# Optimization experiments

Hardware: AMD Instinct MI355X
Metric: run time of the kernel (lower is better)

## Reference

```python
import jax, jax.numpy as jnp
import numpy as np

B, S, H = 64, 2048, 512


def setup_inputs() -> dict:
    key = jax.random.key(0)
    ks = jax.random.split(key, 11)
    sc = 1.0 / np.sqrt(H)
    return {
        "encoder_output": jax.random.normal(ks[0], (B, S, H), jnp.float32),
        "decoder_hidden": jax.random.normal(ks[1], (B, H), jnp.float32),
        "coverage": jax.random.uniform(ks[2], (B, S), jnp.float32),
        # params (torch Linear: y = x @ W.T + b); we store W already transposed as [in, out]
        "Wh": jax.random.normal(ks[3], (H, H), jnp.float32) * sc,
        "bh": jax.random.normal(ks[4], (H,), jnp.float32) * sc,
        "Ws": jax.random.normal(ks[5], (H, H), jnp.float32) * sc,
        "bs": jax.random.normal(ks[6], (H,), jnp.float32) * sc,
        "Wc": jax.random.normal(ks[7], (1, H), jnp.float32) * sc,  # Linear(1, H)
        "bc": jax.random.normal(ks[8], (H,), jnp.float32) * sc,
        "v_w": jax.random.normal(ks[9], (H,), jnp.float32) * sc,   # Linear(H, 1) weight
        "v_b": jax.random.normal(ks[10], (1,), jnp.float32) * sc,
    }


def reference(encoder_output, decoder_hidden, coverage, Wh, bh, Ws, bs, Wc, bc, v_w, v_b):
    # encoder_feature: [B,S,H]
    enc_f = jnp.einsum('bsh,hk->bsk', encoder_output, Wh) + bh
    # decoder_feature: [B,1,H]
    dec_f = (decoder_hidden @ Ws + bs)[:, None, :]
    # coverage_feature: [B,S,H] = cov[...,None] @ Wc(1,H) + bc
    cov_f = coverage[:, :, None] * Wc[0] + bc
    feat = jnp.tanh(enc_f + dec_f + cov_f)          # [B,S,H]
    e_t = jnp.einsum('bsh,h->bs', feat, v_w) + v_b[0]  # [B,S]
    a_t = jax.nn.softmax(e_t, axis=-1)
    sum_coverage = coverage + a_t
    return a_t, sum_coverage
```

## Files before the change

kernel.cpp:

```cpp
#include <hip/hip_runtime.h>
#include <math.h>


#define B_ 64
#define S_ 2048
#define H_ 512
#define M_ (B_ * S_)

#define RPB 128
#define BN 64
#define NPH 8

typedef __attribute__((ext_vector_type(4))) float f32x4;
typedef __attribute__((ext_vector_type(8))) short s16x8;

__device__ __forceinline__ short f2bf(float f) {
    unsigned u = __float_as_uint(f);
    u += 0x7fffu + ((u >> 16) & 1u);
    return (short)(u >> 16);
}

__device__ __forceinline__ s16x8 cvt8(float4 a, float4 b) {
    s16x8 r;
    r[0] = f2bf(a.x); r[1] = f2bf(a.y); r[2] = f2bf(a.z); r[3] = f2bf(a.w);
    r[4] = f2bf(b.x); r[5] = f2bf(b.y); r[6] = f2bf(b.z); r[7] = f2bf(b.w);
    return r;
}

__device__ __forceinline__ float fast_tanh(float x) {
    return 1.0f - 2.0f / (__expf(2.0f * x) + 1.0f);
}

__global__ __launch_bounds__(256) void transpose_cast(
    const float* __restrict__ Wh, short* __restrict__ Bt) {
    __shared__ float tile[32][33];
    const int n0 = blockIdx.x * 32, k0 = blockIdx.y * 32;
    const int tx = threadIdx.x & 31, ty = threadIdx.x >> 5;
#pragma unroll
    for (int r = 0; r < 32; r += 8)
        tile[ty + r][tx] = Wh[(size_t)(k0 + ty + r) * H_ + n0 + tx];
    __syncthreads();
#pragma unroll
    for (int r = 0; r < 32; r += 8)
        Bt[(size_t)(n0 + ty + r) * H_ + k0 + tx] = f2bf(tile[tx][ty + r]);
}

__global__ __launch_bounds__(512) void dec_kernel(
    const float* __restrict__ dh, const float* __restrict__ Ws,
    const float* __restrict__ bs, const float* __restrict__ bh,
    const float* __restrict__ bc, float* __restrict__ D) {
    const int b = blockIdx.x;
    const int h = threadIdx.x;
    __shared__ float sdh[H_];
    sdh[h] = dh[b * H_ + h];
    __syncthreads();
    float acc = bs[h] + bh[h] + bc[h];
#pragma unroll 8
    for (int k = 0; k < H_; ++k)
        acc = fmaf(sdh[k], Ws[k * H_ + h], acc);
    D[b * H_ + h] = acc;
}

__global__ __launch_bounds__(256, 2) void gemm_fused(
    const float* __restrict__ A,
    const short* __restrict__ Bt,
    const float* __restrict__ cover,
    const float* __restrict__ Wc,
    const float* __restrict__ vw,
    const float* __restrict__ D,
    float* __restrict__ e_t) {
    __shared__ __align__(16) short Bs[BN * H_];

    const int tid = threadIdx.x;
    const int w = tid >> 6;
    const int l = tid & 63;
    const int q = l >> 4;
    const int ml = l & 15;

    const int row_blk = blockIdx.x * RPB;
    const int b = row_blk >> 11;
    const int r0 = row_blk + w * 32;

    s16x8 a[2][16];
    {
        const float* ap = A + (size_t)(r0 + ml) * H_ + q * 8;
#pragma unroll
        for (int kw = 0; kw < 16; ++kw) {
#pragma unroll
            for (int t = 0; t < 2; ++t) {
                const float* p = ap + (size_t)t * 16 * H_ + kw * 32;
                float4 x = *(const float4*)p;
                float4 y = *(const float4*)(p + 4);
                a[t][kw] = cvt8(x, y);
            }
        }
    }

    float cv[2][4];
#pragma unroll
    for (int t = 0; t < 2; ++t)
#pragma unroll
        for (int r = 0; r < 4; ++r)
            cv[t][r] = cover[r0 + t * 16 + q * 4 + r];

    const int sn = tid >> 2;
    const int sq = tid & 3;
    const int sv = sn >> 4;
    const int sml = sn & 15;
    short* sdst0 = Bs + sv * 512 + (sq * 16 + (sml ^ (sq << 1))) * 8;
    const int fb = (q * 16 + (ml ^ (q << 1))) * 8;

    float ecur[2][4] = {};

    for (int ph = 0; ph < NPH; ++ph) {
        const short* sg = Bt + ((size_t)ph * BN + sn) * H_ + sq * 8;
        if (ph) __syncthreads();
#pragma unroll
        for (int hv = 0; hv < 2; ++hv) {
            s16x8 tmp[8];
#pragma unroll
            for (int j = 0; j < 8; ++j)
                tmp[j] = *(const s16x8*)(sg + (hv * 8 + j) * 32);
#pragma unroll
            for (int j = 0; j < 8; ++j)
                *(s16x8*)(sdst0 + (size_t)(hv * 8 + j) * 2048) = tmp[j];
        }
        __syncthreads();

        float wc[4], vv[4], dd[4];
#pragma unroll
        for (int v = 0; v < 4; ++v) {
            const int n = ph * BN + v * 16 + ml;
            wc[v] = Wc[n];
            vv[v] = vw[n];
            dd[v] = D[b * H_ + n];
        }

        f32x4 acc[2][4];
#pragma unroll
        for (int t = 0; t < 2; ++t)
#pragma unroll
            for (int v = 0; v < 4; ++v) acc[t][v] = (f32x4)0.0f;

#pragma unroll
        for (int kw = 0; kw < 16; ++kw) {
            s16x8 bfr[4];
#pragma unroll
            for (int v = 0; v < 4; ++v)
                bfr[v] = *(const s16x8*)&Bs[kw * 2048 + v * 512 + fb];
#pragma unroll
            for (int v = 0; v < 4; ++v) {
                acc[0][v] = __builtin_amdgcn_mfma_f32_16x16x32_bf16(
                    a[0][kw], bfr[v], acc[0][v], 0, 0, 0);
                acc[1][v] = __builtin_amdgcn_mfma_f32_16x16x32_bf16(
                    a[1][kw], bfr[v], acc[1][v], 0, 0, 0);
            }
        }

#pragma unroll
        for (int t = 0; t < 2; ++t) {
#pragma unroll
            for (int v = 0; v < 4; ++v) {
                ecur[t][0] += vv[v] * fast_tanh(acc[t][v].x + fmaf(cv[t][0], wc[v], dd[v]));
                ecur[t][1] += vv[v] * fast_tanh(acc[t][v].y + fmaf(cv[t][1], wc[v], dd[v]));
                ecur[t][2] += vv[v] * fast_tanh(acc[t][v].z + fmaf(cv[t][2], wc[v], dd[v]));
                ecur[t][3] += vv[v] * fast_tanh(acc[t][v].w + fmaf(cv[t][3], wc[v], dd[v]));
            }
        }
    }

#pragma unroll
    for (int t = 0; t < 2; ++t) {
        float p0 = ecur[t][0], p1 = ecur[t][1], p2 = ecur[t][2], p3 = ecur[t][3];
#pragma unroll
        for (int s = 1; s < 16; s <<= 1) {
            p0 += __shfl_xor(p0, s, 64);
            p1 += __shfl_xor(p1, s, 64);
            p2 += __shfl_xor(p2, s, 64);
            p3 += __shfl_xor(p3, s, 64);
        }
        if (ml == 0) {
            float4 st = {p0, p1, p2, p3};
            *(float4*)&e_t[r0 + t * 16 + q * 4] = st;
        }
    }
}

__global__ __launch_bounds__(256) void softmax_kernel(
    const float* __restrict__ e_t, const float* __restrict__ cover,
    const float* __restrict__ vb, float* __restrict__ out) {
    const int b = blockIdx.x;
    const int tid = threadIdx.x;
    const float vbv = vb[0];

    float e[8];
    float mx = -1e30f;
#pragma unroll
    for (int r = 0; r < 8; ++r) {
        e[r] = e_t[b * S_ + r * 256 + tid] + vbv;
        mx = fmaxf(mx, e[r]);
    }
#pragma unroll
    for (int off = 32; off >= 1; off >>= 1) mx = fmaxf(mx, __shfl_xor(mx, off, 64));

    __shared__ float sm[4], ss[4], sbc[2];
    const int wid = tid >> 6, lane = tid & 63;
    if (lane == 0) sm[wid] = mx;
    __syncthreads();
    if (tid == 0) sbc[0] = fmaxf(fmaxf(sm[0], sm[1]), fmaxf(sm[2], sm[3]));
    __syncthreads();
    mx = sbc[0];

    float ex[8];
    float sum = 0.0f;
#pragma unroll
    for (int r = 0; r < 8; ++r) {
        ex[r] = __expf(e[r] - mx);
        sum += ex[r];
    }
#pragma unroll
    for (int off = 32; off >= 1; off >>= 1) sum += __shfl_xor(sum, off, 64);
    if (lane == 0) ss[wid] = sum;
    __syncthreads();
    if (tid == 0) sbc[1] = ss[0] + ss[1] + ss[2] + ss[3];
    __syncthreads();
    const float inv = 1.0f / sbc[1];

#pragma unroll
    for (int r = 0; r < 8; ++r) {
        const int s = r * 256 + tid;
        const float a = ex[r] * inv;
        out[b * S_ + s] = a;
        out[M_ + b * S_ + s] = cover[b * S_ + s] + a;
    }
}

extern "C" void kernel_launch(void* const* d_in, const int* in_sizes, int n_in,
                              void* d_out, int out_size, void* d_ws, size_t ws_size,
                              hipStream_t stream) {
    const float* enc = (const float*)d_in[0];
    const float* dh  = (const float*)d_in[1];
    const float* cov = (const float*)d_in[2];
    const float* Wh  = (const float*)d_in[3];
    const float* bh  = (const float*)d_in[4];
    const float* Ws  = (const float*)d_in[5];
    const float* bs  = (const float*)d_in[6];
    const float* Wc  = (const float*)d_in[7];
    const float* bc  = (const float*)d_in[8];
    const float* vw  = (const float*)d_in[9];
    const float* vb  = (const float*)d_in[10];
    float* out = (float*)d_out;

    float* e_t  = (float*)d_ws;
    float* Dws  = e_t + M_;
    short* Whbt = (short*)(Dws + B_ * H_);

    transpose_cast<<<dim3(H_ / 32, H_ / 32), 256, 0, stream>>>(Wh, Whbt);
    dec_kernel<<<B_, 512, 0, stream>>>(dh, Ws, bs, bh, bc, Dws);
    gemm_fused<<<M_ / RPB, 256, 0, stream>>>(enc, Whbt, cov, Wc, vw, Dws, e_t);
    softmax_kernel<<<B_, 256, 0, stream>>>(e_t, cov, vb, out);
}
```

Baseline: 492.4 us.

## Double-buffer weight tiles via direct global-to-LDS DMA with prearranged layout

The transpose kernel now writes the bf16 weights in the exact per-phase fragment order the MFMA loop reads. The GEMM then streams each 32-column phase straight into LDS with global_load_lds, double-buffered so the next phase loads while the current one computes. Blocks become 8 waves of 16 rows each, with launch bounds of 4 blocks per CU, which cuts A-fragment registers and raises occupancy. The decoder matvec is split across two blocks per batch. In exchange there are twice as many phases, each ending in a barrier, and each B fragment is reused by fewer rows.

```diff
diff --git a/kernel.cpp b/kernel.cpp
--- a/kernel.cpp
+++ b/kernel.cpp
@@ -8,11 +8,13 @@
 #define M_ (B_ * S_)
 
 #define RPB 128
-#define BN 64
-#define NPH 8
+#define BN 32
+#define NPH 16
+#define PHB 32768
 
 typedef __attribute__((ext_vector_type(4))) float f32x4;
 typedef __attribute__((ext_vector_type(8))) short s16x8;
+typedef unsigned int u32;
 
 __device__ __forceinline__ short f2bf(float f) {
     unsigned u = __float_as_uint(f);
@@ -31,8 +33,14 @@
     return 1.0f - 2.0f / (__expf(2.0f * x) + 1.0f);
 }
 
+__device__ __forceinline__ void dma16(const void* g, void* s) {
+    __builtin_amdgcn_global_load_lds(
+        (const __attribute__((address_space(1))) u32*)g,
+        (__attribute__((address_space(3))) u32*)s, 16, 0, 0);
+}
+
 __global__ __launch_bounds__(256) void transpose_cast(
-    const float* __restrict__ Wh, short* __restrict__ Bt) {
+    const float* __restrict__ Wh, short* __restrict__ Bimg) {
     __shared__ float tile[32][33];
     const int n0 = blockIdx.x * 32, k0 = blockIdx.y * 32;
     const int tx = threadIdx.x & 31, ty = threadIdx.x >> 5;
@@ -40,19 +48,27 @@
     for (int r = 0; r < 32; r += 8)
         tile[ty + r][tx] = Wh[(size_t)(k0 + ty + r) * H_ + n0 + tx];
     __syncthreads();
-#pragma unroll
-    for (int r = 0; r < 32; r += 8)
-        Bt[(size_t)(n0 + ty + r) * H_ + k0 + tx] = f2bf(tile[tx][ty + r]);
-}
-
-__global__ __launch_bounds__(512) void dec_kernel(
+    const int kw = k0 >> 5;
+    const int q = tx >> 3, j = tx & 7;
+#pragma unroll
+    for (int r = 0; r < 32; r += 8) {
+        const int n = n0 + ty + r;
+        const int ph = n >> 5, v = (n >> 4) & 1, mln = n & 15;
+        const size_t idx = (size_t)ph * 16384 + (size_t)kw * 1024 + v * 512
+                         + (q * 16 + mln) * 8 + j;
+        Bimg[idx] = f2bf(tile[tx][ty + r]);
+    }
+}
+
+__global__ __launch_bounds__(256) void dec_kernel(
     const float* __restrict__ dh, const float* __restrict__ Ws,
     const float* __restrict__ bs, const float* __restrict__ bh,
     const float* __restrict__ bc, float* __restrict__ D) {
     const int b = blockIdx.x;
-    const int h = threadIdx.x;
+    const int h = blockIdx.y * 256 + threadIdx.x;
     __shared__ float sdh[H_];
-    sdh[h] = dh[b * H_ + h];
+    sdh[threadIdx.x] = dh[b * H_ + threadIdx.x];
+    sdh[threadIdx.x + 256] = dh[b * H_ + threadIdx.x + 256];
     __syncthreads();
     float acc = bs[h] + bh[h] + bc[h];
 #pragma unroll 8
@@ -61,15 +77,15 @@
     D[b * H_ + h] = acc;
 }
 
-__global__ __launch_bounds__(256, 2) void gemm_fused(
+__global__ __launch_bounds__(512, 4) void gemm_fused(
     const float* __restrict__ A,
-    const short* __restrict__ Bt,
+    const short* __restrict__ Bimg,
     const float* __restrict__ cover,
     const float* __restrict__ Wc,
     const float* __restrict__ vw,
     const float* __restrict__ D,
     float* __restrict__ e_t) {
-    __shared__ __align__(16) short Bs[BN * H_];
+    __shared__ __align__(16) short Bs[2][BN * H_];
 
     const int tid = threadIdx.x;
     const int w = tid >> 6;
@@ -79,110 +95,80 @@
 
     const int row_blk = blockIdx.x * RPB;
     const int b = row_blk >> 11;
-    const int r0 = row_blk + w * 32;
-
-    s16x8 a[2][16];
+    const int r0 = row_blk + w * 16;
+
+    {
+        const char* g = (const char*)Bimg + (size_t)(w * 4) * 1024 + l * 16;
+        char* s = (char*)&Bs[0][0] + (w * 4) * 1024;
+#pragma unroll
+        for (int c = 0; c < 4; ++c) dma16(g + c * 1024, s + c * 1024);
+    }
+
+    s16x8 a[16];
     {
         const float* ap = A + (size_t)(r0 + ml) * H_ + q * 8;
 #pragma unroll
         for (int kw = 0; kw < 16; ++kw) {
-#pragma unroll
-            for (int t = 0; t < 2; ++t) {
-                const float* p = ap + (size_t)t * 16 * H_ + kw * 32;
-                float4 x = *(const float4*)p;
-                float4 y = *(const float4*)(p + 4);
-                a[t][kw] = cvt8(x, y);
-            }
-        }
-    }
-
-    float cv[2][4];
-#pragma unroll
-    for (int t = 0; t < 2; ++t)
-#pragma unroll
-        for (int r = 0; r < 4; ++r)
-            cv[t][r] = cover[r0 + t * 16 + q * 4 + r];
-
-    const int sn = tid >> 2;
-    const int sq = tid & 3;
-    const int sv = sn >> 4;
-    const int sml = sn & 15;
-    short* sdst0 = Bs + sv * 512 + (sq * 16 + (sml ^ (sq << 1))) * 8;
-    const int fb = (q * 16 + (ml ^ (q << 1))) * 8;
-
-    float ecur[2][4] = {};
+            float4 x = *(const float4*)(ap + kw * 32);
+            float4 y = *(const float4*)(ap + kw * 32 + 4);
+            a[kw] = cvt8(x, y);
+        }
+    }
+
+    float cv[4];
+#pragma unroll
+    for (int r = 0; r < 4; ++r) cv[r] = cover[r0 + q * 4 + r];
+
+    float ecur[4] = {0.0f, 0.0f, 0.0f, 0.0f};
+
+    __syncthreads();
 
     for (int ph = 0; ph < NPH; ++ph) {
-        const short* sg = Bt + ((size_t)ph * BN + sn) * H_ + sq * 8;
-        if (ph) __syncthreads();
-#pragma unroll
-        for (int hv = 0; hv < 2; ++hv) {
-            s16x8 tmp[8];
-#pragma unroll
-            for (int j = 0; j < 8; ++j)
-                tmp[j] = *(const s16x8*)(sg + (hv * 8 + j) * 32);
-#pragma unroll
-            for (int j = 0; j < 8; ++j)
-                *(s16x8*)(sdst0 + (size_t)(hv * 8 + j) * 2048) = tmp[j];
-        }
+        const int cur = ph & 1;
+
+        if (ph + 1 < NPH) {
+            const char* g = (const char*)Bimg + (size_t)(ph + 1) * PHB
+                          + (size_t)(w * 4) * 1024 + l * 16;
+            char* s = (char*)&Bs[cur ^ 1][0] + (w * 4) * 1024;
+#pragma unroll
+            for (int c = 0; c < 4; ++c) dma16(g + c * 1024, s + c * 1024);
+        }
+
+        const int n0 = ph * BN + ml;
+        const float wc0 = Wc[n0],          wc1 = Wc[n0 + 16];
+        const float vv0 = vw[n0],          vv1 = vw[n0 + 16];
+        const float dd0 = D[b * H_ + n0],  dd1 = D[b * H_ + n0 + 16];
+
+        const short* bp = &Bs[cur][0];
+        f32x4 acc0 = (f32x4)0.0f, acc1 = (f32x4)0.0f;
+#pragma unroll
+        for (int kw = 0; kw < 16; ++kw) {
+            s16x8 b0 = *(const s16x8*)(bp + kw * 1024 + l * 8);
+            s16x8 b1 = *(const s16x8*)(bp + kw * 1024 + 512 + l * 8);
+            acc0 = __builtin_amdgcn_mfma_f32_16x16x32_bf16(a[kw], b0, acc0, 0, 0, 0);
+            acc1 = __builtin_amdgcn_mfma_f32_16x16x32_bf16(a[kw], b1, acc1, 0, 0, 0);
+        }
+
+#pragma unroll
+        for (int r = 0; r < 4; ++r) {
+            ecur[r] += vv0 * fast_tanh(acc0[r] + fmaf(cv[r], wc0, dd0));
+            ecur[r] += vv1 * fast_tanh(acc1[r] + fmaf(cv[r], wc1, dd1));
+        }
+
         __syncthreads();
-
-        float wc[4], vv[4], dd[4];
-#pragma unroll
-        for (int v = 0; v < 4; ++v) {
-            const int n = ph * BN + v * 16 + ml;
-            wc[v] = Wc[n];
-            vv[v] = vw[n];
-            dd[v] = D[b * H_ + n];
-        }
-
-        f32x4 acc[2][4];
-#pragma unroll
-        for (int t = 0; t < 2; ++t)
-#pragma unroll
-            for (int v = 0; v < 4; ++v) acc[t][v] = (f32x4)0.0f;
-
-#pragma unroll
-        for (int kw = 0; kw < 16; ++kw) {
-            s16x8 bfr[4];
-#pragma unroll
-            for (int v = 0; v < 4; ++v)
-                bfr[v] = *(const s16x8*)&Bs[kw * 2048 + v * 512 + fb];
-#pragma unroll
-            for (int v = 0; v < 4; ++v) {
-                acc[0][v] = __builtin_amdgcn_mfma_f32_16x16x32_bf16(
-                    a[0][kw], bfr[v], acc[0][v], 0, 0, 0);
-                acc[1][v] = __builtin_amdgcn_mfma_f32_16x16x32_bf16(
-                    a[1][kw], bfr[v], acc[1][v], 0, 0, 0);
-            }
-        }
-
-#pragma unroll
-        for (int t = 0; t < 2; ++t) {
-#pragma unroll
-            for (int v = 0; v < 4; ++v) {
-                ecur[t][0] += vv[v] * fast_tanh(acc[t][v].x + fmaf(cv[t][0], wc[v], dd[v]));
-                ecur[t][1] += vv[v] * fast_tanh(acc[t][v].y + fmaf(cv[t][1], wc[v], dd[v]));
-                ecur[t][2] += vv[v] * fast_tanh(acc[t][v].z + fmaf(cv[t][2], wc[v], dd[v]));
-                ecur[t][3] += vv[v] * fast_tanh(acc[t][v].w + fmaf(cv[t][3], wc[v], dd[v]));
-            }
-        }
-    }
-
-#pragma unroll
-    for (int t = 0; t < 2; ++t) {
-        float p0 = ecur[t][0], p1 = ecur[t][1], p2 = ecur[t][2], p3 = ecur[t][3];
-#pragma unroll
-        for (int s = 1; s < 16; s <<= 1) {
-            p0 += __shfl_xor(p0, s, 64);
-            p1 += __shfl_xor(p1, s, 64);
-            p2 += __shfl_xor(p2, s, 64);
-            p3 += __shfl_xor(p3, s, 64);
-        }
-        if (ml == 0) {
-            float4 st = {p0, p1, p2, p3};
-            *(float4*)&e_t[r0 + t * 16 + q * 4] = st;
-        }
+    }
+
+    float p0 = ecur[0], p1 = ecur[1], p2 = ecur[2], p3 = ecur[3];
+#pragma unroll
+    for (int s = 1; s < 16; s <<= 1) {
+        p0 += __shfl_xor(p0, s, 64);
+        p1 += __shfl_xor(p1, s, 64);
+        p2 += __shfl_xor(p2, s, 64);
+        p3 += __shfl_xor(p3, s, 64);
+    }
+    if (ml == 0) {
+        float4 st = {p0, p1, p2, p3};
+        *(float4*)&e_t[r0 + q * 4] = st;
     }
 }
 
@@ -256,7 +242,7 @@
     short* Whbt = (short*)(Dws + B_ * H_);
 
     transpose_cast<<<dim3(H_ / 32, H_ / 32), 256, 0, stream>>>(Wh, Whbt);
-    dec_kernel<<<B_, 512, 0, stream>>>(dh, Ws, bs, bh, bc, Dws);
-    gemm_fused<<<M_ / RPB, 256, 0, stream>>>(enc, Whbt, cov, Wc, vw, Dws, e_t);
+    dec_kernel<<<dim3(B_, 2), 256, 0, stream>>>(dh, Ws, bs, bh, bc, Dws);
+    gemm_fused<<<M_ / RPB, 512, 0, stream>>>(enc, Whbt, cov, Wc, vw, Dws, e_t);
     softmax_kernel<<<B_, 256, 0, stream>>>(e_t, cov, vb, out);
 }
```

After: 499.8 us. Within noise of the previous version (+1.5%).
